# Kernel optimization log

Measured on AMD Instinct MI355X. Metric: run time of the kernel, lower is better.

Reference implementation:

```python
import jax, jax.numpy as jnp
import numpy as np
import math

B, S, D, H, L = 16, 1024, 256, 8, 4
OBS, ACT = 160, 96
DH = D // H  # 32, even as required by RoPE
ROPE_BASE = 10000.0
LN_EPS = 1e-5


def setup_inputs() -> dict:
    key = jax.random.key(0)
    ks = jax.random.split(key, 16)
    s = 0.02
    n = jax.random.normal
    return {
        "obs_seq": n(ks[0], (B, S, OBS), jnp.float32),
        "action_seq": n(ks[1], (B, S, ACT), jnp.float32),
        # linears stored as [in, out] (transpose of torch convention)
        "in_W": n(ks[2], (OBS + ACT, D), jnp.float32) * s,
        "in_b": jnp.zeros((D,), jnp.float32),
        "qW": n(ks[3], (L, D, D), jnp.float32) * s,
        "qb": jnp.zeros((L, D), jnp.float32),
        "kW": n(ks[4], (L, D, D), jnp.float32) * s,
        "kb": jnp.zeros((L, D), jnp.float32),
        "vW": n(ks[5], (L, D, D), jnp.float32) * s,
        "vb": jnp.zeros((L, D), jnp.float32),
        "oW": n(ks[6], (L, D, D), jnp.float32) * s,
        "ob": jnp.zeros((L, D), jnp.float32),
        "out_W": n(ks[7], (D, D), jnp.float32) * s,
        "out_b": jnp.zeros((D,), jnp.float32),
        "ln_g": jnp.ones((D,), jnp.float32),
        "ln_b": jnp.zeros((D,), jnp.float32),
    }


def _rope(x):
    # x: [B,H,S,DH]; interleaved real/imag rotation (stride-2 split like torch code)
    pos = jnp.arange(S, dtype=jnp.float32)[:, None]                 # [S,1]
    freq_seq = jnp.arange(0, DH, 2, dtype=jnp.float32)              # [DH/2]
    inv_freq = 1.0 / (ROPE_BASE ** (freq_seq / DH))
    freqs = pos * inv_freq[None, :]                                  # [S,DH/2]
    cos = jnp.cos(freqs)[None, None]                                 # [1,1,S,DH/2]
    sin = jnp.sin(freqs)[None, None]
    xr = x[..., 0::2]
    xi = x[..., 1::2]
    rr = xr * cos - xi * sin
    ri = xr * sin + xi * cos
    # interleave back: [..., DH/2, 2] -> [..., DH]
    return jnp.stack([rr, ri], axis=-1).reshape(x.shape)


def _attn_layer(x, qW, qb, kW, kb, vW, vb, oW, ob):
    def heads(t):
        return t.reshape(B, S, H, DH).transpose(0, 2, 1, 3)  # [B,H,S,DH]
    q = _rope(heads(x @ qW + qb))
    k = _rope(heads(x @ kW + kb))
    v = heads(x @ vW + vb)
    scores = jnp.einsum('bhqd,bhkd->bhqk', q, k) / math.sqrt(DH)
    w = jax.nn.softmax(scores, axis=-1)  # dropout is identity at inference
    o = jnp.einsum('bhqk,bhkd->bhqd', w, v)
    o = o.transpose(0, 2, 1, 3).reshape(B, S, D)
    return o @ oW + ob


def reference(obs_seq, action_seq, in_W, in_b, qW, qb, kW, kb, vW, vb, oW, ob,
              out_W, out_b, ln_g, ln_b):
    x = jnp.concatenate([obs_seq, action_seq], axis=-1) @ in_W + in_b  # [B,S,D]
    for l in range(L):  # residual self-attention stack with RoPE
        x = x + _attn_layer(x, qW[l], qb[l], kW[l], kb[l], vW[l], vb[l], oW[l], ob[l])
    y = x @ out_W + out_b
    mu = jnp.mean(y, axis=-1, keepdims=True)
    var = jnp.mean(jnp.square(y - mu), axis=-1, keepdims=True)
    y = (y - mu) / jnp.sqrt(var + LN_EPS) * ln_g + ln_b
    context_embedding = y[:, -1]       # seq_lengths=None path: last timestep
    sequence_embeddings = y
    return context_embedding, sequence_embeddings
```

## Files before the change

### kernel.cpp

```cpp
#include <hip/hip_runtime.h>
#include <hip/hip_bf16.h>
#include <math.h>

#define B_ 16
#define S_ 1024
#define D_ 256
#define H_ 8
#define L_ 4
#define DH_ 32
#define OBS_ 160
#define ACT_ 96
#define M_ (B_*S_)

typedef __attribute__((ext_vector_type(8)))  short short8v;
typedef __attribute__((ext_vector_type(4)))  short short4v;
typedef __attribute__((ext_vector_type(4)))  float f32x4;
typedef __attribute__((ext_vector_type(4)))  unsigned uint4v;

#define ALPHA_ 0.25507313f

__device__ inline short bf16rne(float x) {
    unsigned u = __builtin_bit_cast(unsigned, x);
    unsigned r = (u + 0x7fffu + ((u >> 16) & 1u)) >> 16;
    return (short)r;
}

#if __has_builtin(__builtin_amdgcn_exp2f)
#define EXP2F(x) __builtin_amdgcn_exp2f(x)
#else
#define EXP2F(x) exp2f(x)
#endif

__device__ inline unsigned cvtpk_bf16(float lo, float hi) {
    unsigned r;
    asm("v_cvt_pk_bf16_f32 %0, %1, %2" : "=v"(r) : "v"(lo), "v"(hi));
    return r;
}

__global__ __launch_bounds__(256) void preproc_k(
    const float* __restrict__ obs, const float* __restrict__ act,
    const float* __restrict__ qW, const float* __restrict__ kW,
    const float* __restrict__ vW, const float* __restrict__ oW,
    const float* __restrict__ outW, const float* __restrict__ inW,
    short* __restrict__ xIn,
    short* __restrict__ WTqkv, short* __restrict__ WTo,
    short* __restrict__ WTf, short* __restrict__ WTin,
    float* __restrict__ cosT2, float* __restrict__ sinT2)
{
    __shared__ float T[64][65];
    const int bid = blockIdx.x;
    const int tid = threadIdx.x;

    if (bid < 288) {
        const int bx = bid & 15, z = bid >> 4;
        const int tr = (bx & 3) * 64, tc = (bx >> 2) * 64;
        const float* src;
        short* dst;
        if (z < 16) {
            int lay = z >> 2, w = z & 3;
            if (w == 0)      { src = qW + lay * 65536; dst = WTqkv + lay * 196608; }
            else if (w == 1) { src = kW + lay * 65536; dst = WTqkv + lay * 196608 + 65536; }
            else if (w == 2) { src = vW + lay * 65536; dst = WTqkv + lay * 196608 + 131072; }
            else             { src = oW + lay * 65536; dst = WTo + lay * 65536; }
        } else if (z == 16) { src = outW; dst = WTf; }
        else                { src = inW;  dst = WTin; }
        #pragma unroll
        for (int it = 0; it < 4; ++it) {
            int r = (tid >> 4) + it * 16, c = (tid & 15) * 4;
            *(float4*)&T[r][c] = *(const float4*)&src[(size_t)(tr + r) * 256 + tc + c];
        }
        __syncthreads();
        #pragma unroll
        for (int it = 0; it < 4; ++it) {
            int n = (tid >> 4) + it * 16, k = (tid & 15) * 4;
            short4v o = {bf16rne(T[k][n]), bf16rne(T[k + 1][n]),
                         bf16rne(T[k + 2][n]), bf16rne(T[k + 3][n])};
            *(short4v*)&dst[(size_t)(tc + n) * 256 + tr + k] = o;
        }
    } else if (bid < 2336) {
        const int idx = ((bid - 288) * 256 + tid) * 8;
        const int row = idx >> 8, col = idx & 255;
        const float* s = (col < OBS_) ? (obs + (size_t)row * OBS_ + col)
                                      : (act + (size_t)row * ACT_ + (col - OBS_));
        const float4 v0 = *(const float4*)s;
        const float4 v1 = *(const float4*)(s + 4);
        short8v o = {bf16rne(v0.x), bf16rne(v0.y), bf16rne(v0.z), bf16rne(v0.w),
                     bf16rne(v1.x), bf16rne(v1.y), bf16rne(v1.z), bf16rne(v1.w)};
        *(short8v*)&xIn[idx] = o;
    } else {
        const int idx = (bid - 2336) * 256 + tid;
        const int i = idx >> 10, s = idx & 1023;
        float invf = powf(10000.0f, -(float)(2 * i) / 32.0f);
        float ang = (float)s * invf;
        float sn, cs;
        sincosf(ang, &sn, &cs);
        cosT2[idx] = cs;
        sinT2[idx] = sn;
    }
}

template<int EPI>
__global__ __launch_bounds__(512, 4) void gemm_k(
    const short* __restrict__ A, const short* __restrict__ WT,
    const float* __restrict__ bq, const float* __restrict__ bk,
    const float* __restrict__ bv,
    float* __restrict__ xF, short* __restrict__ xB,
    short* __restrict__ Q2, short* __restrict__ K2, short* __restrict__ VT,
    float* __restrict__ yF,
    const float* __restrict__ cosT2, const float* __restrict__ sinT2)
{
    __shared__ short As[2][256 * 32];
    __shared__ short Bs[2][64 * 32];
    const int tid = threadIdx.x;
    const int l = tid & 63;
    const int wid = tid >> 6;
    const int wr = wid >> 1, wc = wid & 1;
    const int bm = blockIdx.x * 256, bn = blockIdx.y * 64;

    const short* aSrc0 = A + (size_t)(bm + (tid >> 2)) * 256 + (tid & 3) * 8;
    const short* aSrc1 = aSrc0 + 128 * 256;
    const short* bSrc  = WT + (size_t)(bn + ((tid & 255) >> 2)) * 256 + (tid & 3) * 8;

    {
        short8v a0 = *(const short8v*)aSrc0;
        short8v a1 = *(const short8v*)aSrc1;
        *(short8v*)&As[0][tid * 8]         = a0;
        *(short8v*)&As[0][(tid + 512) * 8] = a1;
        if (tid < 256) {
            short8v b0 = *(const short8v*)bSrc;
            *(short8v*)&Bs[0][tid * 8] = b0;
        }
    }
    __syncthreads();

    f32x4 acc[4][2];
    #pragma unroll
    for (int i = 0; i < 4; ++i)
        #pragma unroll
        for (int j = 0; j < 2; ++j) acc[i][j] = (f32x4){0.f, 0.f, 0.f, 0.f};

    #pragma unroll
    for (int t = 0; t < 8; ++t) {
        const int cur = t & 1;
        short8v na0, na1, nb;
        if (t < 7) {
            const int k = (t + 1) * 32;
            na0 = *(const short8v*)&aSrc0[k];
            na1 = *(const short8v*)&aSrc1[k];
            if (tid < 256) nb = *(const short8v*)&bSrc[k];
        }
        short8v af[4], bf[2];
        #pragma unroll
        for (int i = 0; i < 4; ++i)
            af[i] = *(const short8v*)&As[cur][(wr * 64 + i * 16 + (l & 15)) * 32 + (l >> 4) * 8];
        #pragma unroll
        for (int j = 0; j < 2; ++j)
            bf[j] = *(const short8v*)&Bs[cur][(wc * 32 + j * 16 + (l & 15)) * 32 + (l >> 4) * 8];
        #pragma unroll
        for (int i = 0; i < 4; ++i)
            #pragma unroll
            for (int j = 0; j < 2; ++j)
                acc[i][j] = __builtin_amdgcn_mfma_f32_16x16x32_bf16(af[i], bf[j], acc[i][j], 0, 0, 0);
        if (t < 7) {
            const int nxt = cur ^ 1;
            *(short8v*)&As[nxt][tid * 8]         = na0;
            *(short8v*)&As[nxt][(tid + 512) * 8] = na1;
            if (tid < 256) *(short8v*)&Bs[nxt][tid * 8] = nb;
            __syncthreads();
        }
    }

    if (EPI == 0) {
        const int region = bn >> 8;
        if (region == 2) {
            #pragma unroll
            for (int i = 0; i < 4; ++i) {
                const int m0 = bm + wr * 64 + i * 16 + ((l >> 4) << 2);
                const int bI = m0 >> 10, s0 = m0 & 1023;
                const int w  = s0 & 31;
                const int sp = (s0 & ~31) | ((((w & 15) >> 2) << 3) | ((w >> 4) << 2));
                #pragma unroll
                for (int j = 0; j < 2; ++j) {
                    const int nl = (bn & 255) + wc * 32 + j * 16 + (l & 15);
                    const float bb = bv[nl];
                    const f32x4 v = acc[i][j];
                    const int h = nl >> 5, dhh = nl & 31;
                    short4v o = {bf16rne(v[0] + bb), bf16rne(v[1] + bb),
                                 bf16rne(v[2] + bb), bf16rne(v[3] + bb)};
                    *(short4v*)&VT[((size_t)((bI * 8 + h) * 32 + dhh) << 10) + sp] = o;
                }
            }
        } else {
            const float* bias = (region == 0) ? bq : bk;
            __syncthreads();
            short* scr = &As[0][0];
            #pragma unroll
            for (int i = 0; i < 4; ++i) {
                const int tl0 = wr * 64 + i * 16 + ((l >> 4) << 2);
                const int s0r = (bm + tl0) & 1023;
                #pragma unroll
                for (int j = 0; j < 2; ++j) {
                    const int ncl = wc * 32 + j * 16 + (l & 15);
                    const int nl = (bn & 255) + ncl;
                    const float bb = bias[nl];
                    f32x4 v = acc[i][j];
                    v[0] += bb; v[1] += bb; v[2] += bb; v[3] += bb;
                    if (region == 0) { v *= ALPHA_; }
                    const int ir = (nl & 31) >> 1;
                    const f32x4 cs = *(const f32x4*)&cosT2[ir * 1024 + s0r];
                    const f32x4 sn = *(const f32x4*)&sinT2[ir * 1024 + s0r];
                    f32x4 pr;
                    #pragma unroll
                    for (int c = 0; c < 4; ++c) pr[c] = __shfl_xor(v[c], 1);
                    const float sg = (nl & 1) ? 1.f : -1.f;
                    #pragma unroll
                    for (int c = 0; c < 4; ++c)
                        v[c] = v[c] * cs[c] + sg * pr[c] * sn[c];
                    #pragma unroll
                    for (int c = 0; c < 4; ++c) {
                        const int tl = tl0 + c;
                        const int pos = (((ncl >> 3) ^ (tl & 7)) << 3) | (ncl & 7);
                        scr[tl * 64 + pos] = bf16rne(v[c]);
                    }
                }
            }
            __syncthreads();
            const int r = tid >> 1, h2 = tid & 1;
            const int tok = bm + r;
            const int bI = tok >> 10, s0 = tok & 1023;
            const int hh = ((bn & 255) >> 5) + h2;
            short* dst = ((region == 0) ? Q2 : K2)
                         + ((size_t)((bI * 8 + hh) * 1024 + s0)) * 32;
            #pragma unroll
            for (int k = 0; k < 4; ++k) {
                const int pos = ((h2 * 4 + k) ^ (r & 7)) << 3;
                *(uint4*)&dst[k * 8] = *(const uint4*)&scr[r * 64 + pos];
            }
        }
    } else {
        #pragma unroll
        for (int i = 0; i < 4; ++i) {
            const int m0 = bm + wr * 64 + i * 16 + ((l >> 4) << 2);
            #pragma unroll
            for (int j = 0; j < 2; ++j) {
                const int nn = bn + wc * 32 + j * 16 + (l & 15);
                const float bb = bq[nn];
                const f32x4 v = acc[i][j];
                #pragma unroll
                for (int c = 0; c < 4; ++c) {
                    float rr = v[c] + bb;
                    const size_t off = (size_t)(m0 + c) * 256 + nn;
                    if (EPI == 1) rr += xF[off];
                    if (EPI == 3) {
                        yF[off] = rr;
                    } else {
                        xF[off] = rr;
                        xB[off] = bf16rne(rr);
                    }
                }
            }
        }
    }
}

__global__ __launch_bounds__(512, 2) void attn_k(
    const short* __restrict__ Q2, const short* __restrict__ K2,
    const short* __restrict__ VT, short* __restrict__ O)
{
    __shared__ short lb[65536];
    const int tid = threadIdx.x;
    const int l = tid & 63, wid = tid >> 6;
    const int head = blockIdx.x & 127;
    const int qh = blockIdx.x >> 7;
    const int q0w = qh * 512 + wid * 64;
    const int lq = l & 15, g = l >> 4;

    const short* Kh = K2 + (size_t)head * 32768;
    const short* Vh = VT + (size_t)head * 32768;

    #pragma unroll
    for (int i = 0; i < 8; ++i) {
        const int c = tid + i * 512;
        short8v kv = *(const short8v*)(Kh + c * 8);
        const int key = c >> 2, dc = c & 3;
        *(short8v*)((char*)lb + key * 64 + ((dc ^ ((key >> 1) & 3)) << 4)) = kv;
        short8v vv = *(const short8v*)(Vh + c * 8);
        const int dh = c >> 7, kc = c & 127;
        *(short8v*)((char*)lb + 65536 + (kc >> 2) * 2048 + dh * 64
                    + (((kc & 3) ^ ((dh >> 1) & 3)) << 4)) = vv;
    }

    const short* qp = Q2 + ((size_t)head * 1024 + q0w + lq) * 32 + g * 8;
    const short8v QfA = *(const short8v*)qp;
    const short8v QfB = *(const short8v*)(qp + 512);
    const short8v QfC = *(const short8v*)(qp + 1024);
    const short8v QfD = *(const short8v*)(qp + 1536);

    const char* LBK = (const char*)lb + lq * 64 + ((g ^ ((lq >> 1) & 3)) << 4);
    const char* LBV = LBK + 65536;

    f32x4 aA0 = {0.f,0.f,0.f,0.f}, aA1 = {0.f,0.f,0.f,0.f};
    f32x4 aB0 = {0.f,0.f,0.f,0.f}, aB1 = {0.f,0.f,0.f,0.f};
    f32x4 aC0 = {0.f,0.f,0.f,0.f}, aC1 = {0.f,0.f,0.f,0.f};
    f32x4 aD0 = {0.f,0.f,0.f,0.f}, aD1 = {0.f,0.f,0.f,0.f};
    const f32x4 z4 = {0.f, 0.f, 0.f, 0.f};
    float lsA = 0.f, lsB = 0.f, lsC = 0.f, lsD = 0.f;

    __syncthreads();

#define QSTEP(QF, A0, A1, LS) do {                                             \
        f32x4 s0 = __builtin_amdgcn_mfma_f32_16x16x32_bf16(Kf0, QF, z4, 0,0,0);\
        f32x4 s1 = __builtin_amdgcn_mfma_f32_16x16x32_bf16(Kf1, QF, z4, 0,0,0);\
        float p0 = EXP2F(s0[0]), p1 = EXP2F(s0[1]);                            \
        float p2 = EXP2F(s0[2]), p3 = EXP2F(s0[3]);                            \
        float p4 = EXP2F(s1[0]), p5 = EXP2F(s1[1]);                            \
        float p6 = EXP2F(s1[2]), p7 = EXP2F(s1[3]);                            \
        LS += ((p0 + p1) + (p2 + p3)) + ((p4 + p5) + (p6 + p7));               \
        uint4v pv = {cvtpk_bf16(p0, p1), cvtpk_bf16(p2, p3),                   \
                     cvtpk_bf16(p4, p5), cvtpk_bf16(p6, p7)};                  \
        short8v Pf = __builtin_bit_cast(short8v, pv);                          \
        A0 = __builtin_amdgcn_mfma_f32_16x16x32_bf16(Vf0, Pf, A0, 0,0,0);      \
        A1 = __builtin_amdgcn_mfma_f32_16x16x32_bf16(Vf1, Pf, A1, 0,0,0);      \
    } while (0)

    #pragma unroll 4
    for (int t = 0; t < 32; ++t) {
        const short8v Kf0 = *(const short8v*)(LBK + t * 2048);
        const short8v Kf1 = *(const short8v*)(LBK + t * 2048 + 1024);
        const short8v Vf0 = *(const short8v*)(LBV + t * 2048);
        const short8v Vf1 = *(const short8v*)(LBV + t * 2048 + 1024);
        QSTEP(QfA, aA0, aA1, lsA);
        QSTEP(QfB, aB0, aB1, lsB);
        QSTEP(QfC, aC0, aC1, lsC);
        QSTEP(QfD, aD0, aD1, lsD);
    }
#undef QSTEP

    lsA += __shfl_xor(lsA, 16); lsA += __shfl_xor(lsA, 32);
    lsB += __shfl_xor(lsB, 16); lsB += __shfl_xor(lsB, 32);
    lsC += __shfl_xor(lsC, 16); lsC += __shfl_xor(lsC, 32);
    lsD += __shfl_xor(lsD, 16); lsD += __shfl_xor(lsD, 32);
    const int bI = head >> 3, hh = head & 7;
    short* op = O + ((size_t)(bI * 1024 + q0w + lq)) * 256 + hh * 32 + g * 4;
#define QOUT(A0, A1, LS, ROFF) do {                                            \
        const float inv = 1.f / (LS);                                          \
        short4v o0 = {bf16rne(A0[0] * inv), bf16rne(A0[1] * inv),              \
                      bf16rne(A0[2] * inv), bf16rne(A0[3] * inv)};             \
        short4v o1 = {bf16rne(A1[0] * inv), bf16rne(A1[1] * inv),              \
                      bf16rne(A1[2] * inv), bf16rne(A1[3] * inv)};             \
        *(short4v*)(op + (ROFF) * 256) = o0;                                   \
        *(short4v*)(op + (ROFF) * 256 + 16) = o1;                              \
    } while (0)
    QOUT(aA0, aA1, lsA, 0);
    QOUT(aB0, aB1, lsB, 16);
    QOUT(aC0, aC1, lsC, 32);
    QOUT(aD0, aD1, lsD, 48);
#undef QOUT
}

__global__ __launch_bounds__(256) void ln_k(
    const float* __restrict__ y, const float* __restrict__ g,
    const float* __restrict__ bta, float* __restrict__ outp)
{
    const int tid = threadIdx.x;
    const int wave = tid >> 6, lane = tid & 63;
    const int row = blockIdx.x * 4 + wave;
    const int col = lane * 4;
    float4 t = *(const float4*)&y[(size_t)row * 256 + col];
    float sum = t.x + t.y + t.z + t.w;
    float ss  = t.x * t.x + t.y * t.y + t.z * t.z + t.w * t.w;
    #pragma unroll
    for (int off = 32; off; off >>= 1) {
        sum += __shfl_xor(sum, off);
        ss  += __shfl_xor(ss, off);
    }
    float mean = sum * (1.f / 256.f);
    float var  = ss * (1.f / 256.f) - mean * mean;
    float rstd = rsqrtf(var + 1e-5f);
    float4 gv = *(const float4*)&g[col];
    float4 bv = *(const float4*)&bta[col];
    float4 o;
    o.x = (t.x - mean) * rstd * gv.x + bv.x;
    o.y = (t.y - mean) * rstd * gv.y + bv.y;
    o.z = (t.z - mean) * rstd * gv.z + bv.z;
    o.w = (t.w - mean) * rstd * gv.w + bv.w;
    float* seq = outp + B_ * D_;
    *(float4*)&seq[(size_t)row * 256 + col] = o;
    if ((row & (S_ - 1)) == S_ - 1)
        *(float4*)&outp[(size_t)(row >> 10) * 256 + col] = o;
}

extern "C" void kernel_launch(void* const* d_in, const int* in_sizes, int n_in,
                              void* d_out, int out_size, void* d_ws, size_t ws_size,
                              hipStream_t stream)
{
    const float* obs  = (const float*)d_in[0];
    const float* act  = (const float*)d_in[1];
    const float* inW  = (const float*)d_in[2];
    const float* inb  = (const float*)d_in[3];
    const float* qW   = (const float*)d_in[4];
    const float* qb   = (const float*)d_in[5];
    const float* kW   = (const float*)d_in[6];
    const float* kb   = (const float*)d_in[7];
    const float* vW   = (const float*)d_in[8];
    const float* vb   = (const float*)d_in[9];
    const float* oW   = (const float*)d_in[10];
    const float* ob   = (const float*)d_in[11];
    const float* outW = (const float*)d_in[12];
    const float* outb = (const float*)d_in[13];
    const float* lng  = (const float*)d_in[14];
    const float* lnb  = (const float*)d_in[15];
    float* outp = (float*)d_out;

    const size_t MD = (size_t)M_ * D_;
    float* xF    = (float*)d_ws;
    short* xB    = (short*)(xF + MD);
    short* xIn   = xB + MD;
    short* Q2    = xIn + MD;
    short* K2    = Q2 + MD;
    short* VT    = K2 + MD;
    short* Obf   = VT + MD;
    short* WTqkv = Obf + MD;
    short* WTo   = WTqkv + 786432;
    short* WTf   = WTo + 262144;
    short* WTin  = WTf + 65536;
    float* cosT2 = (float*)(WTin + 65536);
    float* sinT2 = cosT2 + 16384;
    float* ybuf  = (float*)Q2;

    preproc_k<<<2400, 256, 0, stream>>>(obs, act, qW, kW, vW, oW, outW, inW,
                                        xIn, WTqkv, WTo, WTf, WTin, cosT2, sinT2);

    gemm_k<2><<<dim3(64, 4), 512, 0, stream>>>(xIn, WTin, inb, nullptr, nullptr,
            xF, xB, nullptr, nullptr, nullptr, nullptr, nullptr, nullptr);

    for (int lay = 0; lay < L_; ++lay) {
        gemm_k<0><<<dim3(64, 12), 512, 0, stream>>>(xB, WTqkv + lay * 196608,
                qb + lay * 256, kb + lay * 256, vb + lay * 256,
                nullptr, nullptr, Q2, K2, VT, nullptr, cosT2, sinT2);
        attn_k<<<256, 512, 0, stream>>>(Q2, K2, VT, Obf);
        gemm_k<1><<<dim3(64, 4), 512, 0, stream>>>(Obf, WTo + lay * 65536,
                ob + lay * 256, nullptr, nullptr, xF, xB,
                nullptr, nullptr, nullptr, nullptr, nullptr, nullptr);
    }

    gemm_k<3><<<dim3(64, 4), 512, 0, stream>>>(xB, WTf, outb, nullptr, nullptr,
            nullptr, nullptr, nullptr, nullptr, nullptr, ybuf, nullptr, nullptr);
    ln_k<<<M_ / 4, 256, 0, stream>>>(ybuf, lng, lnb, outp);
}
```

Baseline: 282.9 us.

## Shrink GEMM M-tile for narrow GEMMs, transpose Q layout, MFMA row-sum

Templates the GEMM on M-tile rows so the D-output GEMMs (input, out-proj, final) use 128-row tiles and twice as many blocks, which improves occupancy across CUs for these small-N launches. Q is now written transposed, like V, directly from registers, avoiding the LDS scratch path; attention gathers Q with strided scalar loads. The softmax denominator is computed by an extra MFMA against a ones vector instead of VALU adds and shuffles. Scalar strided Q loads and the extra MFMA per step add cost in exchange.

```diff
diff --git a/kernel.cpp b/kernel.cpp
--- a/kernel.cpp
+++ b/kernel.cpp
@@ -99,7 +99,7 @@
     }
 }
 
-template<int EPI>
+template<int EPI, int IB>
 __global__ __launch_bounds__(512, 4) void gemm_k(
     const short* __restrict__ A, const short* __restrict__ WT,
     const float* __restrict__ bq, const float* __restrict__ bk,
@@ -115,7 +115,7 @@
     const int l = tid & 63;
     const int wid = tid >> 6;
     const int wr = wid >> 1, wc = wid & 1;
-    const int bm = blockIdx.x * 256, bn = blockIdx.y * 64;
+    const int bm = blockIdx.x * (IB * 64), bn = blockIdx.y * 64;
 
     const short* aSrc0 = A + (size_t)(bm + (tid >> 2)) * 256 + (tid & 3) * 8;
     const short* aSrc1 = aSrc0 + 128 * 256;
@@ -123,9 +123,11 @@
 
     {
         short8v a0 = *(const short8v*)aSrc0;
-        short8v a1 = *(const short8v*)aSrc1;
-        *(short8v*)&As[0][tid * 8]         = a0;
-        *(short8v*)&As[0][(tid + 512) * 8] = a1;
+        *(short8v*)&As[0][tid * 8] = a0;
+        if (IB == 4) {
+            short8v a1 = *(const short8v*)aSrc1;
+            *(short8v*)&As[0][(tid + 512) * 8] = a1;
+        }
         if (tid < 256) {
             short8v b0 = *(const short8v*)bSrc;
             *(short8v*)&Bs[0][tid * 8] = b0;
@@ -133,9 +135,9 @@
     }
     __syncthreads();
 
-    f32x4 acc[4][2];
+    f32x4 acc[IB][2];
     #pragma unroll
-    for (int i = 0; i < 4; ++i)
+    for (int i = 0; i < IB; ++i)
         #pragma unroll
         for (int j = 0; j < 2; ++j) acc[i][j] = (f32x4){0.f, 0.f, 0.f, 0.f};
 
@@ -146,25 +148,25 @@
         if (t < 7) {
             const int k = (t + 1) * 32;
             na0 = *(const short8v*)&aSrc0[k];
-            na1 = *(const short8v*)&aSrc1[k];
+            if (IB == 4) na1 = *(const short8v*)&aSrc1[k];
             if (tid < 256) nb = *(const short8v*)&bSrc[k];
         }
-        short8v af[4], bf[2];
-        #pragma unroll
-        for (int i = 0; i < 4; ++i)
-            af[i] = *(const short8v*)&As[cur][(wr * 64 + i * 16 + (l & 15)) * 32 + (l >> 4) * 8];
+        short8v af[IB], bf[2];
+        #pragma unroll
+        for (int i = 0; i < IB; ++i)
+            af[i] = *(const short8v*)&As[cur][(wr * (IB * 16) + i * 16 + (l & 15)) * 32 + (l >> 4) * 8];
         #pragma unroll
         for (int j = 0; j < 2; ++j)
             bf[j] = *(const short8v*)&Bs[cur][(wc * 32 + j * 16 + (l & 15)) * 32 + (l >> 4) * 8];
         #pragma unroll
-        for (int i = 0; i < 4; ++i)
+        for (int i = 0; i < IB; ++i)
             #pragma unroll
             for (int j = 0; j < 2; ++j)
                 acc[i][j] = __builtin_amdgcn_mfma_f32_16x16x32_bf16(af[i], bf[j], acc[i][j], 0, 0, 0);
         if (t < 7) {
             const int nxt = cur ^ 1;
-            *(short8v*)&As[nxt][tid * 8]         = na0;
-            *(short8v*)&As[nxt][(tid + 512) * 8] = na1;
+            *(short8v*)&As[nxt][tid * 8] = na0;
+            if (IB == 4) *(short8v*)&As[nxt][(tid + 512) * 8] = na1;
             if (tid < 256) *(short8v*)&Bs[nxt][tid * 8] = nb;
             __syncthreads();
         }
@@ -172,40 +174,56 @@
 
     if (EPI == 0) {
         const int region = bn >> 8;
-        if (region == 2) {
+        if (region != 1) {
             #pragma unroll
-            for (int i = 0; i < 4; ++i) {
-                const int m0 = bm + wr * 64 + i * 16 + ((l >> 4) << 2);
+            for (int i = 0; i < IB; ++i) {
+                const int m0 = bm + wr * (IB * 16) + i * 16 + ((l >> 4) << 2);
                 const int bI = m0 >> 10, s0 = m0 & 1023;
-                const int w  = s0 & 31;
-                const int sp = (s0 & ~31) | ((((w & 15) >> 2) << 3) | ((w >> 4) << 2));
+                int sp = s0;
+                if (region == 2) {
+                    const int w = s0 & 31;
+                    sp = (s0 & ~31) | ((((w & 15) >> 2) << 3) | ((w >> 4) << 2));
+                }
                 #pragma unroll
                 for (int j = 0; j < 2; ++j) {
                     const int nl = (bn & 255) + wc * 32 + j * 16 + (l & 15);
-                    const float bb = bv[nl];
-                    const f32x4 v = acc[i][j];
+                    const float bb = (region == 2) ? bv[nl] : bq[nl];
+                    f32x4 v = acc[i][j];
+                    v[0] += bb; v[1] += bb; v[2] += bb; v[3] += bb;
+                    if (region == 0) {
+                        v *= ALPHA_;
+                        const int ir = (nl & 31) >> 1;
+                        const f32x4 cs = *(const f32x4*)&cosT2[ir * 1024 + s0];
+                        const f32x4 sn = *(const f32x4*)&sinT2[ir * 1024 + s0];
+                        f32x4 pr;
+                        #pragma unroll
+                        for (int c = 0; c < 4; ++c) pr[c] = __shfl_xor(v[c], 1);
+                        const float sg = (nl & 1) ? 1.f : -1.f;
+                        #pragma unroll
+                        for (int c = 0; c < 4; ++c)
+                            v[c] = v[c] * cs[c] + sg * pr[c] * sn[c];
+                    }
                     const int h = nl >> 5, dhh = nl & 31;
-                    short4v o = {bf16rne(v[0] + bb), bf16rne(v[1] + bb),
-                                 bf16rne(v[2] + bb), bf16rne(v[3] + bb)};
-                    *(short4v*)&VT[((size_t)((bI * 8 + h) * 32 + dhh) << 10) + sp] = o;
+                    short4v o = {bf16rne(v[0]), bf16rne(v[1]),
+                                 bf16rne(v[2]), bf16rne(v[3])};
+                    short* dst = (region == 2) ? VT : Q2;
+                    *(short4v*)&dst[((size_t)((bI * 8 + h) * 32 + dhh) << 10) + sp] = o;
                 }
             }
         } else {
-            const float* bias = (region == 0) ? bq : bk;
             __syncthreads();
             short* scr = &As[0][0];
             #pragma unroll
-            for (int i = 0; i < 4; ++i) {
-                const int tl0 = wr * 64 + i * 16 + ((l >> 4) << 2);
+            for (int i = 0; i < IB; ++i) {
+                const int tl0 = wr * (IB * 16) + i * 16 + ((l >> 4) << 2);
                 const int s0r = (bm + tl0) & 1023;
                 #pragma unroll
                 for (int j = 0; j < 2; ++j) {
                     const int ncl = wc * 32 + j * 16 + (l & 15);
                     const int nl = (bn & 255) + ncl;
-                    const float bb = bias[nl];
+                    const float bb = bk[nl];
                     f32x4 v = acc[i][j];
                     v[0] += bb; v[1] += bb; v[2] += bb; v[3] += bb;
-                    if (region == 0) { v *= ALPHA_; }
                     const int ir = (nl & 31) >> 1;
                     const f32x4 cs = *(const f32x4*)&cosT2[ir * 1024 + s0r];
                     const f32x4 sn = *(const f32x4*)&sinT2[ir * 1024 + s0r];
@@ -229,8 +247,7 @@
             const int tok = bm + r;
             const int bI = tok >> 10, s0 = tok & 1023;
             const int hh = ((bn & 255) >> 5) + h2;
-            short* dst = ((region == 0) ? Q2 : K2)
-                         + ((size_t)((bI * 8 + hh) * 1024 + s0)) * 32;
+            short* dst = K2 + ((size_t)((bI * 8 + hh) * 1024 + s0)) * 32;
             #pragma unroll
             for (int k = 0; k < 4; ++k) {
                 const int pos = ((h2 * 4 + k) ^ (r & 7)) << 3;
@@ -239,8 +256,8 @@
         }
     } else {
         #pragma unroll
-        for (int i = 0; i < 4; ++i) {
-            const int m0 = bm + wr * 64 + i * 16 + ((l >> 4) << 2);
+        for (int i = 0; i < IB; ++i) {
+            const int m0 = bm + wr * (IB * 16) + i * 16 + ((l >> 4) << 2);
             #pragma unroll
             for (int j = 0; j < 2; ++j) {
                 const int nn = bn + wc * 32 + j * 16 + (l & 15);
@@ -290,11 +307,18 @@
                     + (((kc & 3) ^ ((dh >> 1) & 3)) << 4)) = vv;
     }
 
-    const short* qp = Q2 + ((size_t)head * 1024 + q0w + lq) * 32 + g * 8;
-    const short8v QfA = *(const short8v*)qp;
-    const short8v QfB = *(const short8v*)(qp + 512);
-    const short8v QfC = *(const short8v*)(qp + 1024);
-    const short8v QfD = *(const short8v*)(qp + 1536);
+    const short* qbase = Q2 + (size_t)head * 32768 + q0w + lq;
+    short8v QfA, QfB, QfC, QfD;
+    #pragma unroll
+    for (int j = 0; j < 8; ++j) {
+        const size_t off = (size_t)(g * 8 + j) * 1024;
+        QfA[j] = qbase[off];
+        QfB[j] = qbase[off + 16];
+        QfC[j] = qbase[off + 32];
+        QfD[j] = qbase[off + 48];
+    }
+    const short one = (short)0x3F80;
+    const short8v OnesF = {one, one, one, one, one, one, one, one};
 
     const char* LBK = (const char*)lb + lq * 64 + ((g ^ ((lq >> 1) & 3)) << 4);
     const char* LBV = LBK + 65536;
@@ -303,24 +327,25 @@
     f32x4 aB0 = {0.f,0.f,0.f,0.f}, aB1 = {0.f,0.f,0.f,0.f};
     f32x4 aC0 = {0.f,0.f,0.f,0.f}, aC1 = {0.f,0.f,0.f,0.f};
     f32x4 aD0 = {0.f,0.f,0.f,0.f}, aD1 = {0.f,0.f,0.f,0.f};
+    f32x4 lA = {0.f,0.f,0.f,0.f}, lB = {0.f,0.f,0.f,0.f};
+    f32x4 lC = {0.f,0.f,0.f,0.f}, lD = {0.f,0.f,0.f,0.f};
     const f32x4 z4 = {0.f, 0.f, 0.f, 0.f};
-    float lsA = 0.f, lsB = 0.f, lsC = 0.f, lsD = 0.f;
 
     __syncthreads();
 
-#define QSTEP(QF, A0, A1, LS) do {                                             \
+#define QSTEP(QF, A0, A1, LACC) do {                                           \
         f32x4 s0 = __builtin_amdgcn_mfma_f32_16x16x32_bf16(Kf0, QF, z4, 0,0,0);\
         f32x4 s1 = __builtin_amdgcn_mfma_f32_16x16x32_bf16(Kf1, QF, z4, 0,0,0);\
         float p0 = EXP2F(s0[0]), p1 = EXP2F(s0[1]);                            \
         float p2 = EXP2F(s0[2]), p3 = EXP2F(s0[3]);                            \
         float p4 = EXP2F(s1[0]), p5 = EXP2F(s1[1]);                            \
         float p6 = EXP2F(s1[2]), p7 = EXP2F(s1[3]);                            \
-        LS += ((p0 + p1) + (p2 + p3)) + ((p4 + p5) + (p6 + p7));               \
         uint4v pv = {cvtpk_bf16(p0, p1), cvtpk_bf16(p2, p3),                   \
                      cvtpk_bf16(p4, p5), cvtpk_bf16(p6, p7)};                  \
         short8v Pf = __builtin_bit_cast(short8v, pv);                          \
         A0 = __builtin_amdgcn_mfma_f32_16x16x32_bf16(Vf0, Pf, A0, 0,0,0);      \
         A1 = __builtin_amdgcn_mfma_f32_16x16x32_bf16(Vf1, Pf, A1, 0,0,0);      \
+        LACC = __builtin_amdgcn_mfma_f32_16x16x32_bf16(OnesF, Pf, LACC, 0,0,0);\
     } while (0)
 
     #pragma unroll 4
@@ -329,21 +354,17 @@
         const short8v Kf1 = *(const short8v*)(LBK + t * 2048 + 1024);
         const short8v Vf0 = *(const short8v*)(LBV + t * 2048);
         const short8v Vf1 = *(const short8v*)(LBV + t * 2048 + 1024);
-        QSTEP(QfA, aA0, aA1, lsA);
-        QSTEP(QfB, aB0, aB1, lsB);
-        QSTEP(QfC, aC0, aC1, lsC);
-        QSTEP(QfD, aD0, aD1, lsD);
+        QSTEP(QfA, aA0, aA1, lA);
+        QSTEP(QfB, aB0, aB1, lB);
+        QSTEP(QfC, aC0, aC1, lC);
+        QSTEP(QfD, aD0, aD1, lD);
     }
 #undef QSTEP
 
-    lsA += __shfl_xor(lsA, 16); lsA += __shfl_xor(lsA, 32);
-    lsB += __shfl_xor(lsB, 16); lsB += __shfl_xor(lsB, 32);
-    lsC += __shfl_xor(lsC, 16); lsC += __shfl_xor(lsC, 32);
-    lsD += __shfl_xor(lsD, 16); lsD += __shfl_xor(lsD, 32);
     const int bI = head >> 3, hh = head & 7;
     short* op = O + ((size_t)(bI * 1024 + q0w + lq)) * 256 + hh * 32 + g * 4;
-#define QOUT(A0, A1, LS, ROFF) do {                                            \
-        const float inv = 1.f / (LS);                                          \
+#define QOUT(A0, A1, LACC, ROFF) do {                                          \
+        const float inv = 1.f / (LACC)[0];                                     \
         short4v o0 = {bf16rne(A0[0] * inv), bf16rne(A0[1] * inv),              \
                       bf16rne(A0[2] * inv), bf16rne(A0[3] * inv)};             \
         short4v o1 = {bf16rne(A1[0] * inv), bf16rne(A1[1] * inv),              \
@@ -351,10 +372,10 @@
         *(short4v*)(op + (ROFF) * 256) = o0;                                   \
         *(short4v*)(op + (ROFF) * 256 + 16) = o1;                              \
     } while (0)
-    QOUT(aA0, aA1, lsA, 0);
-    QOUT(aB0, aB1, lsB, 16);
-    QOUT(aC0, aC1, lsC, 32);
-    QOUT(aD0, aD1, lsD, 48);
+    QOUT(aA0, aA1, lA, 0);
+    QOUT(aB0, aB1, lB, 16);
+    QOUT(aC0, aC1, lC, 32);
+    QOUT(aD0, aD1, lD, 48);
 #undef QOUT
 }
 
@@ -431,20 +452,20 @@
     preproc_k<<<2400, 256, 0, stream>>>(obs, act, qW, kW, vW, oW, outW, inW,
                                         xIn, WTqkv, WTo, WTf, WTin, cosT2, sinT2);
 
-    gemm_k<2><<<dim3(64, 4), 512, 0, stream>>>(xIn, WTin, inb, nullptr, nullptr,
+    gemm_k<2,2><<<dim3(128, 4), 512, 0, stream>>>(xIn, WTin, inb, nullptr, nullptr,
             xF, xB, nullptr, nullptr, nullptr, nullptr, nullptr, nullptr);
 
     for (int lay = 0; lay < L_; ++lay) {
-        gemm_k<0><<<dim3(64, 12), 512, 0, stream>>>(xB, WTqkv + lay * 196608,
+        gemm_k<0,4><<<dim3(64, 12), 512, 0, stream>>>(xB, WTqkv + lay * 196608,
                 qb + lay * 256, kb + lay * 256, vb + lay * 256,
                 nullptr, nullptr, Q2, K2, VT, nullptr, cosT2, sinT2);
         attn_k<<<256, 512, 0, stream>>>(Q2, K2, VT, Obf);
-        gemm_k<1><<<dim3(64, 4), 512, 0, stream>>>(Obf, WTo + lay * 65536,
+        gemm_k<1,2><<<dim3(128, 4), 512, 0, stream>>>(Obf, WTo + lay * 65536,
                 ob + lay * 256, nullptr, nullptr, xF, xB,
                 nullptr, nullptr, nullptr, nullptr, nullptr, nullptr);
     }
 
-    gemm_k<3><<<dim3(64, 4), 512, 0, stream>>>(xB, WTf, outb, nullptr, nullptr,
+    gemm_k<3,2><<<dim3(128, 4), 512, 0, stream>>>(xB, WTf, outb, nullptr, nullptr,
             nullptr, nullptr, nullptr, nullptr, nullptr, ybuf, nullptr, nullptr);
     ln_k<<<M_ / 4, 256, 0, stream>>>(ybuf, lng, lnb, outp);
 }
```

After: 255.4 us. 9.7% less time.
